# Optimization experiments

Hardware: AMD Instinct MI355X
Metric: run time of the kernel (lower is better)

Reference implementation:

```python
import jax, jax.numpy as jnp
import numpy as np

USER_NUM = 100000
ITEM_NUM = 100000
DIM = 64
BS = 256


def setup_inputs() -> dict:
    key = jax.random.key(0)
    k1, k2, k3, k4, k5 = jax.random.split(key, 5)
    # xavier_normal-ish scale for embeddings/linear
    user_table = jax.random.normal(k1, (USER_NUM, DIM), dtype=jnp.float32) * 0.1
    item_table = jax.random.normal(k2, (ITEM_NUM, DIM), dtype=jnp.float32) * 0.1
    cls_w = jax.random.normal(k3, (5, DIM), dtype=jnp.float32) * (2.0 / (DIM + 5)) ** 0.5
    cls_b = jnp.zeros((5,), dtype=jnp.float32)
    batch_user = jax.random.randint(k4, (BS,), 0, USER_NUM, dtype=jnp.int64)
    values = jnp.array([[1.0, 2.0, 3.0, 4.0, 5.0]], dtype=jnp.float32)
    return {
        "batch_user": batch_user,
        "user_table": user_table,
        "item_table": item_table,
        "cls_w": cls_w,
        "cls_b": cls_b,
        "values": values,
    }


def reference(batch_user, user_table, item_table, cls_w, cls_b, values):
    # forward_full_items: score every (user, item) pair.
    # Torch materializes h_ui = (u repeated) * (items tiled) of shape
    # [bs*item_num, dim]; mathematically logits = einsum over dim, so we
    # fuse the broadcasted product with the tiny Linear to avoid the
    # huge expanded intermediate while computing identical math.
    u = user_table[batch_user]                       # [bs, dim]
    # logits[b,i,c] = sum_d u[b,d] * item[i,d] * W[c,d] + b[c]
    logits = jnp.einsum('bd,id,cd->bic', u, item_table, cls_w) + cls_b  # [bs, item_num, 5]
    prob = jax.nn.softmax(logits, axis=-1)
    return jnp.sum(prob * values[0], axis=-1)        # [bs, item_num]
```

## Files before the change

### kernel.cpp

```cpp
#include <hip/hip_runtime.h>

#define I_TOTAL 100000
#define DIM 64
#define BS 256

typedef __attribute__((ext_vector_type(8))) short bf16x8;
typedef __attribute__((ext_vector_type(4))) float f32x4;

__device__ inline unsigned short f2bf(float x) {
    union { float f; unsigned u; } v; v.f = x;
    return (unsigned short)((v.u + 0x8000u) >> 16);
}

__global__ __launch_bounds__(256) void prep_M(
    const int* __restrict__ bu, const float* __restrict__ ut,
    const float* __restrict__ cw, unsigned short* __restrict__ Mbf)
{
    int idx = blockIdx.x * 256 + threadIdx.x;
    int d = (idx & 15) * 4;
    int n = idx >> 4;
    int c = n >> 8, b = n & 255;
    const float s = 1.4426950408889634f;
    float4 u = *(const float4*)(ut + (long)bu[b] * DIM + d);
    float4 w = *(const float4*)(cw + c * DIM + d);
    ushort4 r;
    r.x = f2bf(u.x * w.x * s);
    r.y = f2bf(u.y * w.y * s);
    r.z = f2bf(u.z * w.z * s);
    r.w = f2bf(u.w * w.w * s);
    *(ushort4*)(Mbf + n * DIM + d) = r;
}

__global__ __launch_bounds__(256) void conv_items(
    const float* __restrict__ item, unsigned short* __restrict__ itbf)
{
    long t = (long)blockIdx.x * 256 + threadIdx.x;
    const float4* p = (const float4*)(item + t * 8);
    float4 a = p[0], b = p[1];
    ushort4 r0, r1;
    r0.x = f2bf(a.x); r0.y = f2bf(a.y); r0.z = f2bf(a.z); r0.w = f2bf(a.w);
    r1.x = f2bf(b.x); r1.y = f2bf(b.y); r1.z = f2bf(b.z); r1.w = f2bf(b.w);
    ushort4* q = (ushort4*)(itbf + t * 8);
    q[0] = r0; q[1] = r1;
}

__global__ __launch_bounds__(256) void gemm_softmax(
    const unsigned short* __restrict__ itbf,
    const unsigned short* __restrict__ Mbf,
    const float* __restrict__ clsb, const float* __restrict__ vals,
    float* __restrict__ out)
{
    __shared__ float ldsb[4224];

    const int blk = blockIdx.x;
    const int r8 = blk & 7;
    const int q  = blk >> 3;
    const int g  = q & 15;
    const int a  = q >> 4;
    const int y  = a * 8 + r8;
    if (y >= 98) return;

    const int lane = threadIdx.x & 63;
    const int wave = threadIdx.x >> 6;
    const int col  = lane & 15;
    const int quad = lane >> 4;

    const int b_base = g * 16;
    const int i_base = y * 1024 + wave * 256;

    bf16x8 afr[5][2];
#pragma unroll
    for (int c = 0; c < 5; ++c) {
        const unsigned short* p = Mbf + (c * BS + b_base + col) * DIM + quad * 8;
        afr[c][0] = *(const bf16x8*)p;
        afr[c][1] = *(const bf16x8*)(p + 32);
    }

    const f32x4 zero = (f32x4){0.f, 0.f, 0.f, 0.f};
    const float s = 1.4426950408889634f;
    float bb[5], vv[5];
#pragma unroll
    for (int c = 0; c < 5; ++c) { bb[c] = clsb[c] * s; vv[c] = vals[c]; }

    if (y < 97) {
        float* wlds = ldsb + wave * 1056 + quad * 264 + col;
        const float* rlds = ldsb + wave * 1056 + quad * 264 + 4 * col;

        float* op[4];
#pragma unroll
        for (int k = 0; k < 4; ++k)
            op[k] = out + (size_t)(b_base + quad * 4 + k) * I_TOTAL + (i_base + 4 * col);

        const unsigned short* bp = itbf + (size_t)(i_base + col) * DIM + quad * 8;

#pragma unroll 1
        for (int t4 = 0; t4 < 4; ++t4) {
#pragma unroll
            for (int ti = 0; ti < 4; ++ti) {
                bf16x8 b0 = *(const bf16x8*)(bp + ti * 1024);
                bf16x8 b1 = *(const bf16x8*)(bp + ti * 1024 + 32);
                f32x4 acc[5];
#pragma unroll
                for (int c = 0; c < 5; ++c) {
                    acc[c] = __builtin_amdgcn_mfma_f32_16x16x32_bf16(afr[c][0], b0, zero, 0, 0, 0);
                    acc[c] = __builtin_amdgcn_mfma_f32_16x16x32_bf16(afr[c][1], b1, acc[c], 0, 0, 0);
                }
                f32x4 l[5];
#pragma unroll
                for (int c = 0; c < 5; ++c) l[c] = acc[c] + bb[c];
#pragma unroll
                for (int rr = 0; rr < 4; ++rr) {
                    float e0 = __builtin_amdgcn_exp2f(l[0][rr]);
                    float e1 = __builtin_amdgcn_exp2f(l[1][rr]);
                    float e2 = __builtin_amdgcn_exp2f(l[2][rr]);
                    float e3 = __builtin_amdgcn_exp2f(l[3][rr]);
                    float e4 = __builtin_amdgcn_exp2f(l[4][rr]);
                    float den = ((e0 + e1) + (e2 + e3)) + e4;
                    float num = e0 * vv[0];
                    num = fmaf(e1, vv[1], num);
                    num = fmaf(e2, vv[2], num);
                    num = fmaf(e3, vv[3], num);
                    num = fmaf(e4, vv[4], num);
                    wlds[rr * 64 + ti * 16] = num * __builtin_amdgcn_rcpf(den);
                }
            }
#pragma unroll
            for (int k = 0; k < 4; ++k) {
                f32x4 o4 = *(const f32x4*)(rlds + k * 64);
                *(f32x4*)op[k] = o4;
                op[k] += 64;
            }
            bp += 4 * 1024;
        }
    } else {
#pragma unroll 1
        for (int t = 0; t < 16; ++t) {
            int i  = i_base + t * 16 + col;
            int ic = i < I_TOTAL ? i : I_TOTAL - 1;
            const unsigned short* p2 = itbf + (size_t)ic * DIM + quad * 8;
            bf16x8 b0 = *(const bf16x8*)p2;
            bf16x8 b1 = *(const bf16x8*)(p2 + 32);
            f32x4 acc[5];
#pragma unroll
            for (int c = 0; c < 5; ++c) {
                acc[c] = __builtin_amdgcn_mfma_f32_16x16x32_bf16(afr[c][0], b0, zero, 0, 0, 0);
                acc[c] = __builtin_amdgcn_mfma_f32_16x16x32_bf16(afr[c][1], b1, acc[c], 0, 0, 0);
            }
            if (i < I_TOTAL) {
#pragma unroll
                for (int rr = 0; rr < 4; ++rr) {
                    float e0 = __builtin_amdgcn_exp2f(acc[0][rr] + bb[0]);
                    float e1 = __builtin_amdgcn_exp2f(acc[1][rr] + bb[1]);
                    float e2 = __builtin_amdgcn_exp2f(acc[2][rr] + bb[2]);
                    float e3 = __builtin_amdgcn_exp2f(acc[3][rr] + bb[3]);
                    float e4 = __builtin_amdgcn_exp2f(acc[4][rr] + bb[4]);
                    float den = ((e0 + e1) + (e2 + e3)) + e4;
                    float num = e0 * vv[0];
                    num = fmaf(e1, vv[1], num);
                    num = fmaf(e2, vv[2], num);
                    num = fmaf(e3, vv[3], num);
                    num = fmaf(e4, vv[4], num);
                    out[(size_t)(b_base + quad * 4 + rr) * I_TOTAL + i] =
                        num * __builtin_amdgcn_rcpf(den);
                }
            }
        }
    }
}

__global__ __launch_bounds__(256) void gemm_softmax_fb(
    const float* __restrict__ item, const unsigned short* __restrict__ Mbf,
    const float* __restrict__ clsb, const float* __restrict__ vals,
    float* __restrict__ out)
{
    const int lane = threadIdx.x & 63;
    const int wave = threadIdx.x >> 6;
    const int col  = lane & 15;
    const int quad = lane >> 4;
    const int  b_base = blockIdx.x * 16;
    const long i_wave = (long)blockIdx.y * 256 + wave * 64;

    bf16x8 afr[5][2];
#pragma unroll
    for (int c = 0; c < 5; ++c) {
        const unsigned short* p = Mbf + (c * BS + b_base + col) * DIM + quad * 8;
        afr[c][0] = *(const bf16x8*)p;
        afr[c][1] = *(const bf16x8*)(p + 32);
    }
    f32x4 acc[5][4];
#pragma unroll
    for (int c = 0; c < 5; ++c)
#pragma unroll
        for (int t = 0; t < 4; ++t) acc[c][t] = (f32x4){0.f,0.f,0.f,0.f};
#pragma unroll
    for (int t = 0; t < 4; ++t) {
        long i  = i_wave + t * 16 + col;
        long ic = (i < I_TOTAL) ? i : (I_TOTAL - 1);
        const float4* fp = (const float4*)(item + ic * DIM);
        float4 q0 = fp[2*quad], q1 = fp[2*quad+1], q2 = fp[8+2*quad], q3 = fp[8+2*quad+1];
        bf16x8 b0, b1;
        b0[0]=(short)f2bf(q0.x); b0[1]=(short)f2bf(q0.y); b0[2]=(short)f2bf(q0.z); b0[3]=(short)f2bf(q0.w);
        b0[4]=(short)f2bf(q1.x); b0[5]=(short)f2bf(q1.y); b0[6]=(short)f2bf(q1.z); b0[7]=(short)f2bf(q1.w);
        b1[0]=(short)f2bf(q2.x); b1[1]=(short)f2bf(q2.y); b1[2]=(short)f2bf(q2.z); b1[3]=(short)f2bf(q2.w);
        b1[4]=(short)f2bf(q3.x); b1[5]=(short)f2bf(q3.y); b1[6]=(short)f2bf(q3.z); b1[7]=(short)f2bf(q3.w);
#pragma unroll
        for (int c = 0; c < 5; ++c) {
            acc[c][t] = __builtin_amdgcn_mfma_f32_16x16x32_bf16(afr[c][0], b0, acc[c][t], 0, 0, 0);
            acc[c][t] = __builtin_amdgcn_mfma_f32_16x16x32_bf16(afr[c][1], b1, acc[c][t], 0, 0, 0);
        }
    }
    const float s = 1.4426950408889634f;
    float bb[5], vv[5];
#pragma unroll
    for (int c = 0; c < 5; ++c) { bb[c] = clsb[c] * s; vv[c] = vals[c]; }
#pragma unroll
    for (int t = 0; t < 4; ++t) {
        long i = i_wave + t * 16 + col;
        if (i >= I_TOTAL) continue;
#pragma unroll
        for (int r = 0; r < 4; ++r) {
            int b = b_base + quad * 4 + r;
            float num = 0.f, den = 0.f;
#pragma unroll
            for (int c = 0; c < 5; ++c) {
                float e = __builtin_amdgcn_exp2f(acc[c][t][r] + bb[c]);
                den += e; num = fmaf(e, vv[c], num);
            }
            out[(long)b * I_TOTAL + i] = num * __builtin_amdgcn_rcpf(den);
        }
    }
}

extern "C" void kernel_launch(void* const* d_in, const int* in_sizes, int n_in,
                              void* d_out, int out_size, void* d_ws, size_t ws_size,
                              hipStream_t stream) {
    const int*   bu   = (const int*)d_in[0];
    const float* ut   = (const float*)d_in[1];
    const float* it   = (const float*)d_in[2];
    const float* cw   = (const float*)d_in[3];
    const float* cb   = (const float*)d_in[4];
    const float* vals = (const float*)d_in[5];
    float* out = (float*)d_out;
    unsigned short* Mbf  = (unsigned short*)d_ws;
    unsigned short* itbf = (unsigned short*)((char*)d_ws + 163840);

    const size_t needed = 163840 + (size_t)I_TOTAL * DIM * 2;

    prep_M<<<80, 256, 0, stream>>>(bu, ut, cw, Mbf);
    if (ws_size >= needed) {
        conv_items<<<3125, 256, 0, stream>>>(it, itbf);
        gemm_softmax<<<1664, 256, 0, stream>>>(itbf, Mbf, cb, vals, out);
    } else {
        dim3 grid(16, 391);
        gemm_softmax_fb<<<grid, 256, 0, stream>>>(it, Mbf, cb, vals, out);
    }
}
```

Before: 177.3 us.

## Fuse user-weight prep and item bf16 conversion into single GEMM-softmax kernel

Drops the separate prep_M and conv_items kernels. The main kernel now gathers user rows, multiplies them by classifier weights and packs to bf16 in registers, and converts fp32 item rows to bf16 on load using v_cvt_pk_bf16_f32. The classifier bias is folded into the MFMA accumulator init, which removes a per-element add. This saves two launches and the bf16 workspace write and read-back, but each block now reads fp32 items (twice the bytes) and the item table is re-read by the 16 user-group blocks. It also changes rounding from the manual round-half-up to the hardware convert.

```diff
diff --git a/kernel.cpp b/kernel.cpp
--- a/kernel.cpp
+++ b/kernel.cpp
@@ -7,46 +7,24 @@
 typedef __attribute__((ext_vector_type(8))) short bf16x8;
 typedef __attribute__((ext_vector_type(4))) float f32x4;
 
-__device__ inline unsigned short f2bf(float x) {
-    union { float f; unsigned u; } v; v.f = x;
-    return (unsigned short)((v.u + 0x8000u) >> 16);
+__device__ inline unsigned pk_bf16(float lo, float hi) {
+    unsigned r;
+    asm("v_cvt_pk_bf16_f32 %0, %1, %2" : "=v"(r) : "v"(lo), "v"(hi));
+    return r;
 }
 
-__global__ __launch_bounds__(256) void prep_M(
-    const int* __restrict__ bu, const float* __restrict__ ut,
-    const float* __restrict__ cw, unsigned short* __restrict__ Mbf)
-{
-    int idx = blockIdx.x * 256 + threadIdx.x;
-    int d = (idx & 15) * 4;
-    int n = idx >> 4;
-    int c = n >> 8, b = n & 255;
-    const float s = 1.4426950408889634f;
-    float4 u = *(const float4*)(ut + (long)bu[b] * DIM + d);
-    float4 w = *(const float4*)(cw + c * DIM + d);
-    ushort4 r;
-    r.x = f2bf(u.x * w.x * s);
-    r.y = f2bf(u.y * w.y * s);
-    r.z = f2bf(u.z * w.z * s);
-    r.w = f2bf(u.w * w.w * s);
-    *(ushort4*)(Mbf + n * DIM + d) = r;
+__device__ inline bf16x8 pack8(float4 a, float4 b) {
+    union { unsigned u[4]; bf16x8 v; } r;
+    r.u[0] = pk_bf16(a.x, a.y);
+    r.u[1] = pk_bf16(a.z, a.w);
+    r.u[2] = pk_bf16(b.x, b.y);
+    r.u[3] = pk_bf16(b.z, b.w);
+    return r.v;
 }
 
-__global__ __launch_bounds__(256) void conv_items(
-    const float* __restrict__ item, unsigned short* __restrict__ itbf)
-{
-    long t = (long)blockIdx.x * 256 + threadIdx.x;
-    const float4* p = (const float4*)(item + t * 8);
-    float4 a = p[0], b = p[1];
-    ushort4 r0, r1;
-    r0.x = f2bf(a.x); r0.y = f2bf(a.y); r0.z = f2bf(a.z); r0.w = f2bf(a.w);
-    r1.x = f2bf(b.x); r1.y = f2bf(b.y); r1.z = f2bf(b.z); r1.w = f2bf(b.w);
-    ushort4* q = (ushort4*)(itbf + t * 8);
-    q[0] = r0; q[1] = r1;
-}
-
-__global__ __launch_bounds__(256) void gemm_softmax(
-    const unsigned short* __restrict__ itbf,
-    const unsigned short* __restrict__ Mbf,
+__global__ __launch_bounds__(256) void gemm_softmax_fused(
+    const int* __restrict__ bu, const float* __restrict__ ut,
+    const float* __restrict__ it, const float* __restrict__ cw,
     const float* __restrict__ clsb, const float* __restrict__ vals,
     float* __restrict__ out)
 {
@@ -54,9 +32,9 @@
 
     const int blk = blockIdx.x;
     const int r8 = blk & 7;
-    const int q  = blk >> 3;
-    const int g  = q & 15;
-    const int a  = q >> 4;
+    const int qq = blk >> 3;
+    const int g  = qq & 15;
+    const int a  = qq >> 4;
     const int y  = a * 8 + r8;
     if (y >= 98) return;
 
@@ -68,19 +46,38 @@
     const int b_base = g * 16;
     const int i_base = y * 1024 + wave * 256;
 
+    const float s = 1.4426950408889634f;
+
+    const float* up = ut + (size_t)bu[b_base + col] * DIM + quad * 8;
+    float4 u0 = *(const float4*)(up);
+    float4 u1 = *(const float4*)(up + 4);
+    float4 u2 = *(const float4*)(up + 32);
+    float4 u3 = *(const float4*)(up + 36);
+    u0.x *= s; u0.y *= s; u0.z *= s; u0.w *= s;
+    u1.x *= s; u1.y *= s; u1.z *= s; u1.w *= s;
+    u2.x *= s; u2.y *= s; u2.z *= s; u2.w *= s;
+    u3.x *= s; u3.y *= s; u3.z *= s; u3.w *= s;
+
     bf16x8 afr[5][2];
+    f32x4 cin[5];
+    float vv[5];
 #pragma unroll
     for (int c = 0; c < 5; ++c) {
-        const unsigned short* p = Mbf + (c * BS + b_base + col) * DIM + quad * 8;
-        afr[c][0] = *(const bf16x8*)p;
-        afr[c][1] = *(const bf16x8*)(p + 32);
+        const float* wp = cw + c * DIM + quad * 8;
+        float4 w0 = *(const float4*)(wp);
+        float4 w1 = *(const float4*)(wp + 4);
+        float4 w2 = *(const float4*)(wp + 32);
+        float4 w3 = *(const float4*)(wp + 36);
+        float4 m0 = make_float4(u0.x*w0.x, u0.y*w0.y, u0.z*w0.z, u0.w*w0.w);
+        float4 m1 = make_float4(u1.x*w1.x, u1.y*w1.y, u1.z*w1.z, u1.w*w1.w);
+        float4 m2 = make_float4(u2.x*w2.x, u2.y*w2.y, u2.z*w2.z, u2.w*w2.w);
+        float4 m3 = make_float4(u3.x*w3.x, u3.y*w3.y, u3.z*w3.z, u3.w*w3.w);
+        afr[c][0] = pack8(m0, m1);
+        afr[c][1] = pack8(m2, m3);
+        float bc = clsb[c] * s;
+        cin[c] = (f32x4){bc, bc, bc, bc};
+        vv[c] = vals[c];
     }
-
-    const f32x4 zero = (f32x4){0.f, 0.f, 0.f, 0.f};
-    const float s = 1.4426950408889634f;
-    float bb[5], vv[5];
-#pragma unroll
-    for (int c = 0; c < 5; ++c) { bb[c] = clsb[c] * s; vv[c] = vals[c]; }
 
     if (y < 97) {
         float* wlds = ldsb + wave * 1056 + quad * 264 + col;
@@ -91,30 +88,32 @@
         for (int k = 0; k < 4; ++k)
             op[k] = out + (size_t)(b_base + quad * 4 + k) * I_TOTAL + (i_base + 4 * col);
 
-        const unsigned short* bp = itbf + (size_t)(i_base + col) * DIM + quad * 8;
+        const float* bp = it + (size_t)(i_base + col) * DIM + quad * 8;
 
 #pragma unroll 1
         for (int t4 = 0; t4 < 4; ++t4) {
 #pragma unroll
             for (int ti = 0; ti < 4; ++ti) {
-                bf16x8 b0 = *(const bf16x8*)(bp + ti * 1024);
-                bf16x8 b1 = *(const bf16x8*)(bp + ti * 1024 + 32);
+                const float* p = bp + ti * 1024;
+                float4 q0 = *(const float4*)(p);
+                float4 q1 = *(const float4*)(p + 4);
+                float4 q2 = *(const float4*)(p + 32);
+                float4 q3 = *(const float4*)(p + 36);
+                bf16x8 b0 = pack8(q0, q1);
+                bf16x8 b1 = pack8(q2, q3);
                 f32x4 acc[5];
 #pragma unroll
                 for (int c = 0; c < 5; ++c) {
-                    acc[c] = __builtin_amdgcn_mfma_f32_16x16x32_bf16(afr[c][0], b0, zero, 0, 0, 0);
+                    acc[c] = __builtin_amdgcn_mfma_f32_16x16x32_bf16(afr[c][0], b0, cin[c], 0, 0, 0);
                     acc[c] = __builtin_amdgcn_mfma_f32_16x16x32_bf16(afr[c][1], b1, acc[c], 0, 0, 0);
                 }
-                f32x4 l[5];
-#pragma unroll
-                for (int c = 0; c < 5; ++c) l[c] = acc[c] + bb[c];
 #pragma unroll
                 for (int rr = 0; rr < 4; ++rr) {
-                    float e0 = __builtin_amdgcn_exp2f(l[0][rr]);
-                    float e1 = __builtin_amdgcn_exp2f(l[1][rr]);
-                    float e2 = __builtin_amdgcn_exp2f(l[2][rr]);
-                    float e3 = __builtin_amdgcn_exp2f(l[3][rr]);
-                    float e4 = __builtin_amdgcn_exp2f(l[4][rr]);
+                    float e0 = __builtin_amdgcn_exp2f(acc[0][rr]);
+                    float e1 = __builtin_amdgcn_exp2f(acc[1][rr]);
+                    float e2 = __builtin_amdgcn_exp2f(acc[2][rr]);
+                    float e3 = __builtin_amdgcn_exp2f(acc[3][rr]);
+                    float e4 = __builtin_amdgcn_exp2f(acc[4][rr]);
                     float den = ((e0 + e1) + (e2 + e3)) + e4;
                     float num = e0 * vv[0];
                     num = fmaf(e1, vv[1], num);
@@ -137,23 +136,27 @@
         for (int t = 0; t < 16; ++t) {
             int i  = i_base + t * 16 + col;
             int ic = i < I_TOTAL ? i : I_TOTAL - 1;
-            const unsigned short* p2 = itbf + (size_t)ic * DIM + quad * 8;
-            bf16x8 b0 = *(const bf16x8*)p2;
-            bf16x8 b1 = *(const bf16x8*)(p2 + 32);
+            const float* p2 = it + (size_t)ic * DIM + quad * 8;
+            float4 q0 = *(const float4*)(p2);
+            float4 q1 = *(const float4*)(p2 + 4);
+            float4 q2 = *(const float4*)(p2 + 32);
+            float4 q3 = *(const float4*)(p2 + 36);
+            bf16x8 b0 = pack8(q0, q1);
+            bf16x8 b1 = pack8(q2, q3);
             f32x4 acc[5];
 #pragma unroll
             for (int c = 0; c < 5; ++c) {
-                acc[c] = __builtin_amdgcn_mfma_f32_16x16x32_bf16(afr[c][0], b0, zero, 0, 0, 0);
+                acc[c] = __builtin_amdgcn_mfma_f32_16x16x32_bf16(afr[c][0], b0, cin[c], 0, 0, 0);
                 acc[c] = __builtin_amdgcn_mfma_f32_16x16x32_bf16(afr[c][1], b1, acc[c], 0, 0, 0);
             }
             if (i < I_TOTAL) {
 #pragma unroll
                 for (int rr = 0; rr < 4; ++rr) {
-                    float e0 = __builtin_amdgcn_exp2f(acc[0][rr] + bb[0]);
-                    float e1 = __builtin_amdgcn_exp2f(acc[1][rr] + bb[1]);
-                    float e2 = __builtin_amdgcn_exp2f(acc[2][rr] + bb[2]);
-                    float e3 = __builtin_amdgcn_exp2f(acc[3][rr] + bb[3]);
-                    float e4 = __builtin_amdgcn_exp2f(acc[4][rr] + bb[4]);
+                    float e0 = __builtin_amdgcn_exp2f(acc[0][rr]);
+                    float e1 = __builtin_amdgcn_exp2f(acc[1][rr]);
+                    float e2 = __builtin_amdgcn_exp2f(acc[2][rr]);
+                    float e3 = __builtin_amdgcn_exp2f(acc[3][rr]);
+                    float e4 = __builtin_amdgcn_exp2f(acc[4][rr]);
                     float den = ((e0 + e1) + (e2 + e3)) + e4;
                     float num = e0 * vv[0];
                     num = fmaf(e1, vv[1], num);
@@ -168,69 +171,6 @@
     }
 }
 
-__global__ __launch_bounds__(256) void gemm_softmax_fb(
-    const float* __restrict__ item, const unsigned short* __restrict__ Mbf,
-    const float* __restrict__ clsb, const float* __restrict__ vals,
-    float* __restrict__ out)
-{
-    const int lane = threadIdx.x & 63;
-    const int wave = threadIdx.x >> 6;
-    const int col  = lane & 15;
-    const int quad = lane >> 4;
-    const int  b_base = blockIdx.x * 16;
-    const long i_wave = (long)blockIdx.y * 256 + wave * 64;
-
-    bf16x8 afr[5][2];
-#pragma unroll
-    for (int c = 0; c < 5; ++c) {
-        const unsigned short* p = Mbf + (c * BS + b_base + col) * DIM + quad * 8;
-        afr[c][0] = *(const bf16x8*)p;
-        afr[c][1] = *(const bf16x8*)(p + 32);
-    }
-    f32x4 acc[5][4];
-#pragma unroll
-    for (int c = 0; c < 5; ++c)
-#pragma unroll
-        for (int t = 0; t < 4; ++t) acc[c][t] = (f32x4){0.f,0.f,0.f,0.f};
-#pragma unroll
-    for (int t = 0; t < 4; ++t) {
-        long i  = i_wave + t * 16 + col;
-        long ic = (i < I_TOTAL) ? i : (I_TOTAL - 1);
-        const float4* fp = (const float4*)(item + ic * DIM);
-        float4 q0 = fp[2*quad], q1 = fp[2*quad+1], q2 = fp[8+2*quad], q3 = fp[8+2*quad+1];
-        bf16x8 b0, b1;
-        b0[0]=(short)f2bf(q0.x); b0[1]=(short)f2bf(q0.y); b0[2]=(short)f2bf(q0.z); b0[3]=(short)f2bf(q0.w);
-        b0[4]=(short)f2bf(q1.x); b0[5]=(short)f2bf(q1.y); b0[6]=(short)f2bf(q1.z); b0[7]=(short)f2bf(q1.w);
-        b1[0]=(short)f2bf(q2.x); b1[1]=(short)f2bf(q2.y); b1[2]=(short)f2bf(q2.z); b1[3]=(short)f2bf(q2.w);
-        b1[4]=(short)f2bf(q3.x); b1[5]=(short)f2bf(q3.y); b1[6]=(short)f2bf(q3.z); b1[7]=(short)f2bf(q3.w);
-#pragma unroll
-        for (int c = 0; c < 5; ++c) {
-            acc[c][t] = __builtin_amdgcn_mfma_f32_16x16x32_bf16(afr[c][0], b0, acc[c][t], 0, 0, 0);
-            acc[c][t] = __builtin_amdgcn_mfma_f32_16x16x32_bf16(afr[c][1], b1, acc[c][t], 0, 0, 0);
-        }
-    }
-    const float s = 1.4426950408889634f;
-    float bb[5], vv[5];
-#pragma unroll
-    for (int c = 0; c < 5; ++c) { bb[c] = clsb[c] * s; vv[c] = vals[c]; }
-#pragma unroll
-    for (int t = 0; t < 4; ++t) {
-        long i = i_wave + t * 16 + col;
-        if (i >= I_TOTAL) continue;
-#pragma unroll
-        for (int r = 0; r < 4; ++r) {
-            int b = b_base + quad * 4 + r;
-            float num = 0.f, den = 0.f;
-#pragma unroll
-            for (int c = 0; c < 5; ++c) {
-                float e = __builtin_amdgcn_exp2f(acc[c][t][r] + bb[c]);
-                den += e; num = fmaf(e, vv[c], num);
-            }
-            out[(long)b * I_TOTAL + i] = num * __builtin_amdgcn_rcpf(den);
-        }
-    }
-}
-
 extern "C" void kernel_launch(void* const* d_in, const int* in_sizes, int n_in,
                               void* d_out, int out_size, void* d_ws, size_t ws_size,
                               hipStream_t stream) {
@@ -241,17 +181,7 @@
     const float* cb   = (const float*)d_in[4];
     const float* vals = (const float*)d_in[5];
     float* out = (float*)d_out;
-    unsigned short* Mbf  = (unsigned short*)d_ws;
-    unsigned short* itbf = (unsigned short*)((char*)d_ws + 163840);
+    (void)d_ws; (void)ws_size; (void)in_sizes; (void)n_in; (void)out_size;
 
-    const size_t needed = 163840 + (size_t)I_TOTAL * DIM * 2;
-
-    prep_M<<<80, 256, 0, stream>>>(bu, ut, cw, Mbf);
-    if (ws_size >= needed) {
-        conv_items<<<3125, 256, 0, stream>>>(it, itbf);
-        gemm_softmax<<<1664, 256, 0, stream>>>(itbf, Mbf, cb, vals, out);
-    } else {
-        dim3 grid(16, 391);
-        gemm_softmax_fb<<<grid, 256, 0, stream>>>(it, Mbf, cb, vals, out);
-    }
+    gemm_softmax_fused<<<1664, 256, 0, stream>>>(bu, ut, it, cw, cb, vals, out);
 }
```

After: 208.6 us. 17.6% more time.
